# Kernel optimization log

Measured on AMD Instinct MI355X. Metric: run time of the kernel, lower is better.

The kernel has to match this reference:

```python
import jax, jax.numpy as jnp
import numpy as np

ALPHA = 0.5      # sklearn Lasso(alpha=0.5)
N_ITERS = 50     # fixed FISTA iterations
N_POWER = 10     # power iterations for Lipschitz estimate


def _soft(x, thr):
    return jnp.sign(x) * jnp.maximum(jnp.abs(x) - thr, 0.0)


def setup_inputs() -> dict:
    key = jax.random.key(0)
    k1, k2 = jax.random.split(key)
    B, n_rx, n_tx, n_carrier = 8, 4, 32, 256
    M = 256
    D = n_rx * n_tx * n_carrier * 2  # 65536
    x = jax.random.normal(k1, (B, n_rx, n_tx, n_carrier, 2), jnp.float32)
    coding_mat = jax.random.normal(k2, (B, M, D), jnp.float32)
    return {"x": x, "coding_mat": coding_mat}


def _lasso_fista(x, coding_mat):
    B = x.shape[0]
    M = coding_mat.shape[1]
    D = coding_mat.shape[2]
    shape = x.shape
    w_true = x.reshape(B, D)                       # (nrx ntx channel complex) flatten
    y = jnp.einsum('bmd,bd->bm', coding_mat, w_true)  # compressed measurements

    # Lipschitz constant of grad of (1/(2M))||y - Aw||^2 via power iteration on A^T A / M
    def power_step(_, v):
        Av = jnp.einsum('bmd,bd->bm', coding_mat, v)
        v = jnp.einsum('bmd,bm->bd', coding_mat, Av)
        return v / (jnp.linalg.norm(v, axis=-1, keepdims=True) + 1e-12)

    v = jnp.full((B, D), 1.0 / np.sqrt(D), dtype=x.dtype)
    v = jax.lax.fori_loop(0, N_POWER, power_step, v)
    Av = jnp.einsum('bmd,bd->bm', coding_mat, v)
    L = jnp.einsum('bm,bm->b', Av, Av) / M        # rayleigh quotient, v unit norm
    L = jax.lax.stop_gradient(L)[:, None]          # [B,1] step-size constant

    w0 = jnp.zeros((B, D), x.dtype)

    def fista_step(carry, _):
        w, z, t = carry
        r = jnp.einsum('bmd,bd->bm', coding_mat, z) - y
        grad = jnp.einsum('bmd,bm->bd', coding_mat, r) / M
        w_new = _soft(z - grad / L, ALPHA / L)
        t_new = 0.5 * (1.0 + jnp.sqrt(1.0 + 4.0 * t * t))
        z_new = w_new + ((t - 1.0) / t_new) * (w_new - w)
        return (w_new, z_new, t_new), None

    (w, _, _), _ = jax.lax.scan(fista_step, (w0, w0, jnp.float32(1.0)), None, length=N_ITERS)
    return w.reshape(shape)


def reference(x, coding_mat):
    return _lasso_fista(x, coding_mat)
```

## Files before the change

kernel.cpp:

```cpp
#include <hip/hip_runtime.h>
#include <hip/hip_fp16.h>
#include <math.h>

#define B 8
#define M 256
#define D 65536

static constexpr float ALPHA = 0.5f;
static constexpr int N_ITERS = 50;
static constexpr int N_POWER = 10;

typedef _Float16 f16x8 __attribute__((ext_vector_type(8)));
typedef float f32x4 __attribute__((ext_vector_type(4)));

__global__ __launch_bounds__(256) void k_conv(const float* __restrict__ A,
                                              __half* __restrict__ Ah) {
    const size_t n8 = (size_t)B * M * D / 8;
    size_t stride = (size_t)gridDim.x * 256;
    for (size_t i = (size_t)blockIdx.x * 256 + threadIdx.x; i < n8; i += stride) {
        float4 f0 = ((const float4*)A)[2 * i];
        float4 f1 = ((const float4*)A)[2 * i + 1];
        union { uint4 u; __half2 h[4]; } o;
        o.h[0] = __floats2half2_rn(f0.x, f0.y);
        o.h[1] = __floats2half2_rn(f0.z, f0.w);
        o.h[2] = __floats2half2_rn(f1.x, f1.y);
        o.h[3] = __floats2half2_rn(f1.z, f1.w);
        ((uint4*)Ah)[i] = o.u;
    }
}

__global__ __launch_bounds__(256) void k_y_u0(const __half* __restrict__ Ah,
                                              const float* __restrict__ x,
                                              float* __restrict__ y,
                                              float* __restrict__ u) {
    int bm = blockIdx.x;
    int b = bm >> 8;
    const uint4* arow = (const uint4*)(Ah + (size_t)bm * D);
    const float4* xrow = (const float4*)(x + (size_t)b * D);
    float sy = 0.f, ss = 0.f;
#pragma unroll 4
    for (int i = threadIdx.x; i < D / 8; i += 256) {
        uint4 a = arow[i];
        const __half2* hp = (const __half2*)&a;
        float4 x0 = xrow[2 * i], x1 = xrow[2 * i + 1];
        float2 f0 = __half22float2(hp[0]);
        float2 f1 = __half22float2(hp[1]);
        float2 f2 = __half22float2(hp[2]);
        float2 f3 = __half22float2(hp[3]);
        sy += f0.x * x0.x + f0.y * x0.y + f1.x * x0.z + f1.y * x0.w +
              f2.x * x1.x + f2.y * x1.y + f3.x * x1.z + f3.y * x1.w;
        ss += f0.x + f0.y + f1.x + f1.y + f2.x + f2.y + f3.x + f3.y;
    }
    __shared__ float sdata[8];
    for (int off = 32; off > 0; off >>= 1) {
        sy += __shfl_down(sy, off, 64);
        ss += __shfl_down(ss, off, 64);
    }
    int lane = threadIdx.x & 63, wid = threadIdx.x >> 6;
    if (lane == 0) { sdata[wid] = sy; sdata[4 + wid] = ss; }
    __syncthreads();
    if (threadIdx.x == 0) {
        y[bm] = sdata[0] + sdata[1] + sdata[2] + sdata[3];
        u[bm] = (sdata[4] + sdata[5] + sdata[6] + sdata[7]) * 0.00390625f;
    }
}

__global__ __launch_bounds__(256) void k_gram_mfma(const __half* __restrict__ Ah,
                                                   float* __restrict__ G) {
    int bx = blockIdx.x;
    int ch = bx & 31;
    int p  = (bx >> 5) % 3;
    int b  = bx / 96;
    const int PI[3] = {0, 0, 128};
    const int PJ[3] = {0, 128, 128};
    int ti = PI[p], tj = PJ[p];
    int k0 = ch * 2048;

    __shared__ __half As[128 * 32];
    __shared__ __half Bs[128 * 32];

    int t = threadIdx.x;
    int w = t >> 6, lane = t & 63;
    int wr = w >> 1, wc = w & 1;

    const __half* Ab = Ah + (size_t)b * M * D;

    int srow = w * 32 + (lane >> 2);
    int scol = (lane & 3) * 8;

    f32x4 acc[4][4];
#pragma unroll
    for (int i = 0; i < 4; ++i)
#pragma unroll
        for (int j = 0; j < 4; ++j)
            acc[i][j] = (f32x4){0.f, 0.f, 0.f, 0.f};

    int frow = lane & 15;
    int koff = (lane >> 4) * 8;

    for (int ks = 0; ks < 2048; ks += 32) {
        __syncthreads();
        {
            const __half* ga0 = Ab + (size_t)(ti + srow) * D + k0 + ks + scol;
            const __half* ga1 = ga0 + (size_t)16 * D;
            const __half* gb0 = Ab + (size_t)(tj + srow) * D + k0 + ks + scol;
            const __half* gb1 = gb0 + (size_t)16 * D;
            __builtin_amdgcn_global_load_lds(
                (const __attribute__((address_space(1))) void*)ga0,
                (__attribute__((address_space(3))) void*)&As[(w * 32) * 32], 16, 0, 0);
            __builtin_amdgcn_global_load_lds(
                (const __attribute__((address_space(1))) void*)ga1,
                (__attribute__((address_space(3))) void*)&As[(w * 32 + 16) * 32], 16, 0, 0);
            __builtin_amdgcn_global_load_lds(
                (const __attribute__((address_space(1))) void*)gb0,
                (__attribute__((address_space(3))) void*)&Bs[(w * 32) * 32], 16, 0, 0);
            __builtin_amdgcn_global_load_lds(
                (const __attribute__((address_space(1))) void*)gb1,
                (__attribute__((address_space(3))) void*)&Bs[(w * 32 + 16) * 32], 16, 0, 0);
        }
        __syncthreads();

        f16x8 aF[4], bF[4];
#pragma unroll
        for (int i = 0; i < 4; ++i)
            aF[i] = *(const f16x8*)&As[(wr * 64 + i * 16 + frow) * 32 + koff];
#pragma unroll
        for (int j = 0; j < 4; ++j)
            bF[j] = *(const f16x8*)&Bs[(wc * 64 + j * 16 + frow) * 32 + koff];
#pragma unroll
        for (int i = 0; i < 4; ++i)
#pragma unroll
            for (int j = 0; j < 4; ++j)
                acc[i][j] = __builtin_amdgcn_mfma_f32_16x16x32_f16(
                    aF[i], bF[j], acc[i][j], 0, 0, 0);
    }

    float* Gb = G + (size_t)b * M * M;
    bool offd = (ti != tj);
    int r0 = (lane >> 4) * 4;
    int c0 = lane & 15;
#pragma unroll
    for (int i = 0; i < 4; ++i)
#pragma unroll
        for (int j = 0; j < 4; ++j)
#pragma unroll
            for (int r = 0; r < 4; ++r) {
                int gi = ti + wr * 64 + i * 16 + r0 + r;
                int gj = tj + wc * 64 + j * 16 + c0;
                float v = acc[i][j][r];
                atomicAdd(&Gb[(size_t)gi * M + gj], v);
                if (offd) atomicAdd(&Gb[(size_t)gj * M + gi], v);
            }
}

__global__ __launch_bounds__(256) void k_power(const float* __restrict__ G,
                                               const float* __restrict__ u0,
                                               float* __restrict__ Lp) {
    int b = blockIdx.x;
    int m = threadIdx.x;
    __shared__ float su[M];
    __shared__ float red[4];
    su[m] = u0[b * M + m];
    __syncthreads();
    const float* Gb = G + (size_t)b * M * M;
    for (int it = 0; it < N_POWER; ++it) {
        float gm = 0.f;
        const float4* grow = (const float4*)(Gb + (size_t)m * M);
#pragma unroll 8
        for (int k = 0; k < M / 4; ++k) {
            float4 g = grow[k];
            gm += g.x * su[4 * k] + g.y * su[4 * k + 1] + g.z * su[4 * k + 2] +
                  g.w * su[4 * k + 3];
        }
        float part = su[m] * gm;
        for (int off = 32; off > 0; off >>= 1) part += __shfl_down(part, off, 64);
        if ((m & 63) == 0) red[m >> 6] = part;
        __syncthreads();
        float n = sqrtf(red[0] + red[1] + red[2] + red[3]);
        float inv = 1.f / (n + 1e-12f);
        su[m] = gm * inv;
        __syncthreads();
    }
    float part = su[m] * su[m];
    for (int off = 32; off > 0; off >>= 1) part += __shfl_down(part, off, 64);
    if ((m & 63) == 0) red[m >> 6] = part;
    __syncthreads();
    if (m == 0) {
        float L = (red[0] + red[1] + red[2] + red[3]) * (1.0f / 256.0f);
        Lp[b * 4 + 0] = L;
        Lp[b * 4 + 1] = 1.0f / (256.0f * L);
        Lp[b * 4 + 2] = ALPHA / L;
    }
}

__global__ __launch_bounds__(256) void k_cstep(const float* __restrict__ spart,
                                               const float* __restrict__ y,
                                               const float* __restrict__ Lp,
                                               float* __restrict__ c) {
    int blk = blockIdx.x;
    int b = blk >> 3;
    int mg = blk & 7;
    int t = threadIdx.x;
    int tm = t & 31;
    int cg = t >> 5;
    int m = mg * 32 + tm;
    const float* sp = spart + (size_t)b * 512 * M + m;
    float s = 0.f;
#pragma unroll 8
    for (int ch = cg; ch < 512; ch += 8)
        s += sp[(size_t)ch * M];
    __shared__ float red[8][32];
    red[cg][tm] = s;
    __syncthreads();
    if (t < 32) {
        float sv = red[0][t] + red[1][t] + red[2][t] + red[3][t] +
                   red[4][t] + red[5][t] + red[6][t] + red[7][t];
        int bm = b * M + mg * 32 + t;
        c[bm] = (sv - y[bm]) * Lp[b * 4 + 1];
    }
}

__global__ __launch_bounds__(256) void k_fista(const __half* __restrict__ Ah,
                                               const float* __restrict__ cc,
                                               const float* __restrict__ Lp,
                                               float* __restrict__ z,
                                               float* __restrict__ w,
                                               float* __restrict__ spart,
                                               float beta) {
    int cid = blockIdx.x;
    int b = cid >> 9;
    int chunk = cid & 511;
    int d0 = chunk << 7;
    int t = threadIdx.x;
    int dj = t & 15;
    int mi = t >> 4;

    __shared__ float sc[M];
    __shared__ float gws[4][16][8];
    __shared__ float znS[128];
    __shared__ float sred[M];

    sc[t] = cc[b * M + t];
    __syncthreads();

    const __half* Ap = Ah + (size_t)b * M * D + (size_t)mi * D + d0 + dj * 8;
    uint4 areg[16];
    float g[8] = {};
#pragma unroll
    for (int s = 0; s < 16; ++s) {
        areg[s] = *(const uint4*)(Ap + (size_t)(s * 16) * D);
        float cm = sc[s * 16 + mi];
        const __half2* hp = (const __half2*)&areg[s];
        float2 f0 = __half22float2(hp[0]);
        float2 f1 = __half22float2(hp[1]);
        float2 f2 = __half22float2(hp[2]);
        float2 f3 = __half22float2(hp[3]);
        g[0] = fmaf(f0.x, cm, g[0]); g[1] = fmaf(f0.y, cm, g[1]);
        g[2] = fmaf(f1.x, cm, g[2]); g[3] = fmaf(f1.y, cm, g[3]);
        g[4] = fmaf(f2.x, cm, g[4]); g[5] = fmaf(f2.y, cm, g[5]);
        g[6] = fmaf(f3.x, cm, g[6]); g[7] = fmaf(f3.y, cm, g[7]);
    }
#pragma unroll
    for (int j = 0; j < 8; ++j) {
        g[j] += __shfl_xor(g[j], 16, 64);
        g[j] += __shfl_xor(g[j], 32, 64);
    }
    int wv = t >> 6;
    if ((t & 63) < 16) {
#pragma unroll
        for (int j = 0; j < 8; ++j) gws[wv][dj][j] = g[j];
    }
    __syncthreads();

    if (t < 128) {
        int ldj = t >> 3, lj = t & 7;
        float gs = gws[0][ldj][lj] + gws[1][ldj][lj] +
                   gws[2][ldj][lj] + gws[3][ldj][lj];
        size_t zi = (size_t)b * D + d0 + t;
        float thr = Lp[b * 4 + 2];
        float zv = z[zi], wold = w[zi];
        float cand = zv - gs;
        float a1 = fabsf(cand) - thr;
        float wn = a1 > 0.f ? copysignf(a1, cand) : 0.f;
        float znv = wn + beta * (wn - wold);
        w[zi] = wn;
        z[zi] = znv;
        znS[t] = znv;
    }
    __syncthreads();

    float zr[8];
    {
        float4 z0 = *(const float4*)&znS[dj * 8];
        float4 z1 = *(const float4*)&znS[dj * 8 + 4];
        zr[0] = z0.x; zr[1] = z0.y; zr[2] = z0.z; zr[3] = z0.w;
        zr[4] = z1.x; zr[5] = z1.y; zr[6] = z1.z; zr[7] = z1.w;
    }
#pragma unroll
    for (int s = 0; s < 16; ++s) {
        const __half2* hp = (const __half2*)&areg[s];
        float2 f0 = __half22float2(hp[0]);
        float2 f1 = __half22float2(hp[1]);
        float2 f2 = __half22float2(hp[2]);
        float2 f3 = __half22float2(hp[3]);
        float p = f0.x * zr[0] + f0.y * zr[1] + f1.x * zr[2] + f1.y * zr[3] +
                  f2.x * zr[4] + f2.y * zr[5] + f3.x * zr[6] + f3.y * zr[7];
        p += __shfl_xor(p, 1, 64);
        p += __shfl_xor(p, 2, 64);
        p += __shfl_xor(p, 4, 64);
        p += __shfl_xor(p, 8, 64);
        if (dj == 0) sred[s * 16 + mi] = p;
    }
    __syncthreads();
    spart[((size_t)b * 512 + chunk) * M + t] = sred[t];
}

extern "C" void kernel_launch(void* const* d_in, const int* in_sizes, int n_in,
                              void* d_out, int out_size, void* d_ws, size_t ws_size,
                              hipStream_t stream) {
    (void)in_sizes; (void)n_in; (void)out_size; (void)ws_size;
    const float* x = (const float*)d_in[0];
    const float* A = (const float*)d_in[1];
    float* w = (float*)d_out;

    __half* Ah = (__half*)d_ws;
    float* ws = (float*)((char*)d_ws + (size_t)B * M * D * sizeof(__half));
    float* y  = ws;
    float* u  = ws + 2048;
    float* Lp = ws + 4096;
    float* c  = ws + 4128;
    float* z  = ws + 8192;
    float* G  = ws + 8192 + 524288;
    float* spart = G;

    hipMemsetAsync(G, 0, (size_t)B * M * M * sizeof(float), stream);
    hipMemsetAsync(z, 0, (size_t)B * D * sizeof(float), stream);
    hipMemsetAsync(w, 0, (size_t)B * D * sizeof(float), stream);

    k_conv<<<16384, 256, 0, stream>>>(A, Ah);
    k_y_u0<<<B * M, 256, 0, stream>>>(Ah, x, y, u);
    k_gram_mfma<<<8 * 3 * 32, 256, 0, stream>>>(Ah, G);
    k_power<<<B, 256, 0, stream>>>(G, u, Lp);

    hipMemsetAsync(spart, 0, (size_t)B * 512 * M * sizeof(float), stream);

    double t = 1.0;
    for (int k = 0; k < N_ITERS; ++k) {
        double tn = 0.5 * (1.0 + sqrt(1.0 + 4.0 * t * t));
        float beta = (float)((t - 1.0) / tn);
        k_cstep<<<64, 256, 0, stream>>>(spart, y, Lp, c);
        k_fista<<<B * 512, 256, 0, stream>>>(Ah, c, Lp, z, w, spart, beta);
        t = tn;
    }
}
```

Before: 3.734 ms.

## Store fp16 coding matrix in chunk-blocked layout for contiguous per-block tiles

The fp16 conversion now writes A in a blocked layout [b][chunk][m][128], so each FISTA block's 256x128 tile is one contiguous 64KB region instead of 256 rows strided by D. The y/u row-sum kernel is split into a per-chunk partial kernel and a reduction kernel to match the new layout, and the gram kernel's addressing is updated. The aim is better DRAM/TLB locality for the 50 memory-bound FISTA passes, at the cost of scattered writes during conversion and one extra launch.

```diff
diff --git a/kernel.cpp b/kernel.cpp
--- a/kernel.cpp
+++ b/kernel.cpp
@@ -5,6 +5,7 @@
 #define B 8
 #define M 256
 #define D 65536
+#define NCH 512
 
 static constexpr float ALPHA = 0.5f;
 static constexpr int N_ITERS = 50;
@@ -13,8 +14,9 @@
 typedef _Float16 f16x8 __attribute__((ext_vector_type(8)));
 typedef float f32x4 __attribute__((ext_vector_type(4)));
 
+
 __global__ __launch_bounds__(256) void k_conv(const float* __restrict__ A,
-                                              __half* __restrict__ Ah) {
+                                              __half* __restrict__ Aht) {
     const size_t n8 = (size_t)B * M * D / 8;
     size_t stride = (size_t)gridDim.x * 256;
     for (size_t i = (size_t)blockIdx.x * 256 + threadIdx.x; i < n8; i += stride) {
@@ -25,56 +27,106 @@
         o.h[1] = __floats2half2_rn(f0.z, f0.w);
         o.h[2] = __floats2half2_rn(f1.x, f1.y);
         o.h[3] = __floats2half2_rn(f1.z, f1.w);
-        ((uint4*)Ah)[i] = o.u;
-    }
-}
-
-__global__ __launch_bounds__(256) void k_y_u0(const __half* __restrict__ Ah,
-                                              const float* __restrict__ x,
-                                              float* __restrict__ y,
-                                              float* __restrict__ u) {
-    int bm = blockIdx.x;
-    int b = bm >> 8;
-    const uint4* arow = (const uint4*)(Ah + (size_t)bm * D);
-    const float4* xrow = (const float4*)(x + (size_t)b * D);
-    float sy = 0.f, ss = 0.f;
-#pragma unroll 4
-    for (int i = threadIdx.x; i < D / 8; i += 256) {
-        uint4 a = arow[i];
+        size_t d8 = i & (D / 8 - 1);
+        size_t m  = (i >> 13) & (M - 1);
+        size_t b  = i >> 21;
+        size_t ch = d8 >> 4;
+        size_t dlo8 = d8 & 15;
+        ((uint4*)Aht)[(((b * NCH + ch) * M + m) << 4) + dlo8] = o.u;
+    }
+}
+
+__global__ __launch_bounds__(256) void k_ypart(const __half* __restrict__ Aht,
+                                               const float* __restrict__ x,
+                                               float* __restrict__ ypart,
+                                               float* __restrict__ upart) {
+    int cid = blockIdx.x;
+    int b = cid >> 9;
+    int ch = cid & (NCH - 1);
+    int t = threadIdx.x;
+    int dj = t & 15;
+    int mi = t >> 4;
+
+    __shared__ float xs[128];
+    __shared__ float sredY[M];
+    __shared__ float sredU[M];
+    if (t < 32)
+        ((float4*)xs)[t] = ((const float4*)(x + (size_t)b * D + ch * 128))[t];
+    __syncthreads();
+
+    float zr[8];
+    {
+        float4 z0 = *(const float4*)&xs[dj * 8];
+        float4 z1 = *(const float4*)&xs[dj * 8 + 4];
+        zr[0] = z0.x; zr[1] = z0.y; zr[2] = z0.z; zr[3] = z0.w;
+        zr[4] = z1.x; zr[5] = z1.y; zr[6] = z1.z; zr[7] = z1.w;
+    }
+
+    const __half* Ap = Aht + (((size_t)b * NCH + ch) * M + mi) * 128 + dj * 8;
+#pragma unroll
+    for (int s = 0; s < 16; ++s) {
+        uint4 a = *(const uint4*)(Ap + (size_t)(s * 16) * 128);
         const __half2* hp = (const __half2*)&a;
-        float4 x0 = xrow[2 * i], x1 = xrow[2 * i + 1];
         float2 f0 = __half22float2(hp[0]);
         float2 f1 = __half22float2(hp[1]);
         float2 f2 = __half22float2(hp[2]);
         float2 f3 = __half22float2(hp[3]);
-        sy += f0.x * x0.x + f0.y * x0.y + f1.x * x0.z + f1.y * x0.w +
-              f2.x * x1.x + f2.y * x1.y + f3.x * x1.z + f3.y * x1.w;
-        ss += f0.x + f0.y + f1.x + f1.y + f2.x + f2.y + f3.x + f3.y;
-    }
-    __shared__ float sdata[8];
-    for (int off = 32; off > 0; off >>= 1) {
-        sy += __shfl_down(sy, off, 64);
-        ss += __shfl_down(ss, off, 64);
-    }
-    int lane = threadIdx.x & 63, wid = threadIdx.x >> 6;
-    if (lane == 0) { sdata[wid] = sy; sdata[4 + wid] = ss; }
-    __syncthreads();
-    if (threadIdx.x == 0) {
-        y[bm] = sdata[0] + sdata[1] + sdata[2] + sdata[3];
-        u[bm] = (sdata[4] + sdata[5] + sdata[6] + sdata[7]) * 0.00390625f;
-    }
-}
-
-__global__ __launch_bounds__(256) void k_gram_mfma(const __half* __restrict__ Ah,
+        float p = f0.x * zr[0] + f0.y * zr[1] + f1.x * zr[2] + f1.y * zr[3] +
+                  f2.x * zr[4] + f2.y * zr[5] + f3.x * zr[6] + f3.y * zr[7];
+        float q = f0.x + f0.y + f1.x + f1.y + f2.x + f2.y + f3.x + f3.y;
+        p += __shfl_xor(p, 1, 64); q += __shfl_xor(q, 1, 64);
+        p += __shfl_xor(p, 2, 64); q += __shfl_xor(q, 2, 64);
+        p += __shfl_xor(p, 4, 64); q += __shfl_xor(q, 4, 64);
+        p += __shfl_xor(p, 8, 64); q += __shfl_xor(q, 8, 64);
+        if (dj == 0) { sredY[s * 16 + mi] = p; sredU[s * 16 + mi] = q; }
+    }
+    __syncthreads();
+    ypart[((size_t)b * NCH + ch) * M + t] = sredY[t];
+    upart[((size_t)b * NCH + ch) * M + t] = sredU[t];
+}
+
+__global__ __launch_bounds__(256) void k_yred(const float* __restrict__ ypart,
+                                              const float* __restrict__ upart,
+                                              float* __restrict__ y,
+                                              float* __restrict__ u) {
+    int blk = blockIdx.x;
+    int b = blk >> 3;
+    int mg = blk & 7;
+    int t = threadIdx.x;
+    int tm = t & 31;
+    int cg = t >> 5;
+    int m = mg * 32 + tm;
+    const float* yp = ypart + (size_t)b * NCH * M + m;
+    const float* up = upart + (size_t)b * NCH * M + m;
+    float sy = 0.f, su = 0.f;
+#pragma unroll 8
+    for (int ch = cg; ch < NCH; ch += 8) {
+        sy += yp[(size_t)ch * M];
+        su += up[(size_t)ch * M];
+    }
+    __shared__ float redY[8][32], redU[8][32];
+    redY[cg][tm] = sy; redU[cg][tm] = su;
+    __syncthreads();
+    if (t < 32) {
+        float vy = 0.f, vu = 0.f;
+#pragma unroll
+        for (int g = 0; g < 8; ++g) { vy += redY[g][t]; vu += redU[g][t]; }
+        int bm = b * M + mg * 32 + t;
+        y[bm] = vy;
+        u[bm] = vu * 0.00390625f;
+    }
+}
+
+__global__ __launch_bounds__(256) void k_gram_mfma(const __half* __restrict__ Aht,
                                                    float* __restrict__ G) {
     int bx = blockIdx.x;
-    int ch = bx & 31;
+    int ch2 = bx & 31;
     int p  = (bx >> 5) % 3;
     int b  = bx / 96;
     const int PI[3] = {0, 0, 128};
     const int PJ[3] = {0, 128, 128};
     int ti = PI[p], tj = PJ[p];
-    int k0 = ch * 2048;
+    int k0 = ch2 * 2048;
 
     __shared__ __half As[128 * 32];
     __shared__ __half Bs[128 * 32];
@@ -83,8 +135,6 @@
     int w = t >> 6, lane = t & 63;
     int wr = w >> 1, wc = w & 1;
 
-    const __half* Ab = Ah + (size_t)b * M * D;
-
     int srow = w * 32 + (lane >> 2);
     int scol = (lane & 3) * 8;
 
@@ -98,13 +148,17 @@
     int frow = lane & 15;
     int koff = (lane >> 4) * 8;
 
+    const size_t bbase = (size_t)b * NCH;
     for (int ks = 0; ks < 2048; ks += 32) {
+        int d = k0 + ks;
+        size_t chb = bbase + (d >> 7);
+        int dlo = d & 127;
         __syncthreads();
         {
-            const __half* ga0 = Ab + (size_t)(ti + srow) * D + k0 + ks + scol;
-            const __half* ga1 = ga0 + (size_t)16 * D;
-            const __half* gb0 = Ab + (size_t)(tj + srow) * D + k0 + ks + scol;
-            const __half* gb1 = gb0 + (size_t)16 * D;
+            const __half* ga0 = Aht + (chb * M + (ti + srow)) * 128 + dlo + scol;
+            const __half* ga1 = ga0 + 16 * 128;
+            const __half* gb0 = Aht + (chb * M + (tj + srow)) * 128 + dlo + scol;
+            const __half* gb1 = gb0 + 16 * 128;
             __builtin_amdgcn_global_load_lds(
                 (const __attribute__((address_space(1))) void*)ga0,
                 (__attribute__((address_space(3))) void*)&As[(w * 32) * 32], 16, 0, 0);
@@ -204,10 +258,10 @@
     int tm = t & 31;
     int cg = t >> 5;
     int m = mg * 32 + tm;
-    const float* sp = spart + (size_t)b * 512 * M + m;
+    const float* sp = spart + (size_t)b * NCH * M + m;
     float s = 0.f;
 #pragma unroll 8
-    for (int ch = cg; ch < 512; ch += 8)
+    for (int ch = cg; ch < NCH; ch += 8)
         s += sp[(size_t)ch * M];
     __shared__ float red[8][32];
     red[cg][tm] = s;
@@ -220,7 +274,7 @@
     }
 }
 
-__global__ __launch_bounds__(256) void k_fista(const __half* __restrict__ Ah,
+__global__ __launch_bounds__(256) void k_fista(const __half* __restrict__ Aht,
                                                const float* __restrict__ cc,
                                                const float* __restrict__ Lp,
                                                float* __restrict__ z,
@@ -229,7 +283,7 @@
                                                float beta) {
     int cid = blockIdx.x;
     int b = cid >> 9;
-    int chunk = cid & 511;
+    int chunk = cid & (NCH - 1);
     int d0 = chunk << 7;
     int t = threadIdx.x;
     int dj = t & 15;
@@ -243,12 +297,12 @@
     sc[t] = cc[b * M + t];
     __syncthreads();
 
-    const __half* Ap = Ah + (size_t)b * M * D + (size_t)mi * D + d0 + dj * 8;
+    const __half* Ap = Aht + (((size_t)b * NCH + chunk) * M + mi) * 128 + dj * 8;
     uint4 areg[16];
     float g[8] = {};
 #pragma unroll
     for (int s = 0; s < 16; ++s) {
-        areg[s] = *(const uint4*)(Ap + (size_t)(s * 16) * D);
+        areg[s] = *(const uint4*)(Ap + (size_t)(s * 16) * 128);
         float cm = sc[s * 16 + mi];
         const __half2* hp = (const __half2*)&areg[s];
         float2 f0 = __half22float2(hp[0]);
@@ -312,7 +366,7 @@
         if (dj == 0) sred[s * 16 + mi] = p;
     }
     __syncthreads();
-    spart[((size_t)b * 512 + chunk) * M + t] = sred[t];
+    spart[((size_t)b * NCH + chunk) * M + t] = sred[t];
 }
 
 extern "C" void kernel_launch(void* const* d_in, const int* in_sizes, int n_in,
@@ -323,7 +377,7 @@
     const float* A = (const float*)d_in[1];
     float* w = (float*)d_out;
 
-    __half* Ah = (__half*)d_ws;
+    __half* Aht = (__half*)d_ws;
     float* ws = (float*)((char*)d_ws + (size_t)B * M * D * sizeof(__half));
     float* y  = ws;
     float* u  = ws + 2048;
@@ -332,24 +386,27 @@
     float* z  = ws + 8192;
     float* G  = ws + 8192 + 524288;
     float* spart = G;
+    float* ypart = spart + (size_t)B * NCH * M;
+    float* upart = ypart + (size_t)B * NCH * M;
 
     hipMemsetAsync(G, 0, (size_t)B * M * M * sizeof(float), stream);
     hipMemsetAsync(z, 0, (size_t)B * D * sizeof(float), stream);
     hipMemsetAsync(w, 0, (size_t)B * D * sizeof(float), stream);
 
-    k_conv<<<16384, 256, 0, stream>>>(A, Ah);
-    k_y_u0<<<B * M, 256, 0, stream>>>(Ah, x, y, u);
-    k_gram_mfma<<<8 * 3 * 32, 256, 0, stream>>>(Ah, G);
+    k_conv<<<16384, 256, 0, stream>>>(A, Aht);
+    k_ypart<<<B * NCH, 256, 0, stream>>>(Aht, x, ypart, upart);
+    k_yred<<<64, 256, 0, stream>>>(ypart, upart, y, u);
+    k_gram_mfma<<<8 * 3 * 32, 256, 0, stream>>>(Aht, G);
     k_power<<<B, 256, 0, stream>>>(G, u, Lp);
 
-    hipMemsetAsync(spart, 0, (size_t)B * 512 * M * sizeof(float), stream);
+    hipMemsetAsync(spart, 0, (size_t)B * NCH * M * sizeof(float), stream);
 
     double t = 1.0;
     for (int k = 0; k < N_ITERS; ++k) {
         double tn = 0.5 * (1.0 + sqrt(1.0 + 4.0 * t * t));
         float beta = (float)((t - 1.0) / tn);
         k_cstep<<<64, 256, 0, stream>>>(spart, y, Lp, c);
-        k_fista<<<B * 512, 256, 0, stream>>>(Ah, c, Lp, z, w, spart, beta);
+        k_fista<<<B * NCH, 256, 0, stream>>>(Aht, c, Lp, z, w, spart, beta);
         t = tn;
     }
 }
```

Measured after the change: 3.707 ms. Within noise of the previous version (-0.7%).
